# Kernel optimization log

Measured on AMD Instinct MI355X. Metric: run time of the kernel, lower is better.

## Reference

```python
import jax, jax.numpy as jnp
import numpy as np

B, S, H, D = 2, 2048, 16, 128

def setup_inputs() -> dict:
    key = jax.random.key(0)
    kq, kk, kv = jax.random.split(key, 3)
    q = jax.random.normal(kq, (B, S, H, D), dtype=jnp.float32)
    k = jax.random.normal(kk, (B, S, H, D), dtype=jnp.float32)
    v = jax.random.normal(kv, (B, S, H, D), dtype=jnp.float32)
    return {"q": q, "k": k, "v": v}

def reference(q, k, v):
    # Flash-attention semantics: layout [B, S, H, D], causal mask,
    # softmax_scale = 1/sqrt(head_dim), no dropout/window/alibi/bias.
    scale = 1.0 / jnp.sqrt(jnp.asarray(q.shape[-1], dtype=q.dtype))
    # scores: [B, H, Sq, Sk]
    scores = jnp.einsum("bqhd,bkhd->bhqk", q, k) * scale
    sq, sk = q.shape[1], k.shape[1]
    causal_mask = jnp.arange(sk)[None, :] <= jnp.arange(sq)[:, None]  # [Sq, Sk]
    scores = jnp.where(causal_mask[None, None, :, :], scores, jnp.finfo(scores.dtype).min)
    probs = jax.nn.softmax(scores, axis=-1)
    out = jnp.einsum("bhqk,bkhd->bqhd", probs, v)
    return out
```

## Files before the change

kernel.cpp:

```cpp
#include <hip/hip_runtime.h>
#include <hip/hip_bf16.h>

namespace {

constexpr int Bn = 2, Sn = 2048, Hn = 16, Dn = 128;
constexpr int QBLK = 128;
constexpr int KVBLK = 32;
constexpr int RS = Hn * Dn;
constexpr float QSCALE = 0.08838834764831845f * 1.4426950408889634f;

constexpr size_t IMG_BYTES = (size_t)Bn * Hn * 64 * 8192;
constexpr size_t WS_NEED   = 2 * IMG_BYTES;

typedef __bf16 bf16x8 __attribute__((ext_vector_type(8)));
typedef __bf16 bf16x4 __attribute__((ext_vector_type(4)));
typedef float  f32x16 __attribute__((ext_vector_type(16)));

__device__ __forceinline__ f32x16 mfma32(bf16x8 a, bf16x8 b, f32x16 c) {
  return __builtin_amdgcn_mfma_f32_32x32x16_bf16(a, b, c, 0, 0, 0);
}
__device__ __forceinline__ unsigned pack2(float a, float b) {
  union { __bf16 h[2]; unsigned u; } r;
  r.h[0] = (__bf16)a; r.h[1] = (__bf16)b;
  return r.u;
}
__device__ __forceinline__ float pair_max(float x, int hi) {
  auto r = __builtin_amdgcn_permlane32_swap(__float_as_uint(x), __float_as_uint(x), false, false);
  const float sw = __uint_as_float(hi ? r[0] : r[1]);
  return fmaxf(x, sw);
}
__device__ __forceinline__ float pair_sum(float x, int hi) {
  auto r = __builtin_amdgcn_permlane32_swap(__float_as_uint(x), __float_as_uint(x), false, false);
  const float sw = __uint_as_float(hi ? r[0] : r[1]);
  return x + sw;
}
__device__ __forceinline__ float f4e(const float4& v, int j) {
  return j == 0 ? v.x : j == 1 ? v.y : j == 2 ? v.z : v.w;
}
__device__ __forceinline__ float lane_bcast(int row, float v) {
  return __uint_as_float(__builtin_amdgcn_ds_bpermute(row * 4, __float_as_uint(v)));
}

__device__ __forceinline__ void cp16(const char* g, char* l) {
  __builtin_amdgcn_global_load_lds(
      (const __attribute__((address_space(1))) void*)g,
      (__attribute__((address_space(3))) void*)l, 16, 0, 0);
}

__device__ __forceinline__ void dma_barrier() {
  __builtin_amdgcn_sched_barrier(0);
  asm volatile("s_waitcnt vmcnt(0) lgkmcnt(0)" ::: "memory");
  __builtin_amdgcn_s_barrier();
  __builtin_amdgcn_sched_barrier(0);
}
__device__ __forceinline__ void pipeline_barrier() {
  __builtin_amdgcn_sched_barrier(0);
  asm volatile("s_waitcnt lgkmcnt(0)" ::: "memory");
  __builtin_amdgcn_s_barrier();
  __builtin_amdgcn_sched_barrier(0);
}

__global__ __launch_bounds__(256)
void prep_kv(const float* __restrict__ K, const float* __restrict__ V,
             __bf16* __restrict__ KI, __bf16* __restrict__ VI)
{
  const int gid  = (int)blockIdx.x * 256 + (int)threadIdx.x;
  const int half = gid >> 20;
  const int id   = gid & ((1 << 20) - 1);
  const int chunk = id >> 9;
  const int rem   = id & 511;
  const int bh = chunk >> 6, c = chunk & 63;
  const int b = bh >> 4, h = bh & 15;
  if (half == 0) {
    const int key = rem >> 4, dblk = rem & 15;
    const float* src = K + ((size_t)b * Sn + (size_t)c * 32 + key) * RS + h * Dn + dblk * 8;
    float4 a  = *(const float4*)src;
    float4 c2 = *(const float4*)(src + 4);
    bf16x8 f;
    f[0] = (__bf16)a.x;  f[1] = (__bf16)a.y;  f[2] = (__bf16)a.z;  f[3] = (__bf16)a.w;
    f[4] = (__bf16)c2.x; f[5] = (__bf16)c2.y; f[6] = (__bf16)c2.z; f[7] = (__bf16)c2.w;
    char* dst = (char*)KI + (size_t)chunk * 8192 + ((key * 256 + dblk * 16) ^ ((key & 7) << 4));
    *(bf16x8*)dst = f;
  } else {
    const int d = rem >> 2, koct = rem & 3;
    const float* src = V + ((size_t)b * Sn + (size_t)c * 32 + koct * 8) * RS + h * Dn + d;
    bf16x8 f;
#pragma unroll
    for (int j = 0; j < 8; ++j) f[j] = (__bf16)src[(size_t)j * RS];
    const int off = (d * 64 + koct * 16) ^ ((d & 3) << 4) ^ (((d >> 3) & 1) << 6);
    *(bf16x8*)((char*)VI + (size_t)chunk * 8192 + off) = f;
  }
}

__global__ __launch_bounds__(512)
void fa_fwd_dma(const float* __restrict__ Q, const __bf16* __restrict__ KI,
                const __bf16* __restrict__ VI, float* __restrict__ O)
{
  __shared__ __align__(16) __bf16 Klds[4][4096];
  __shared__ __align__(16) __bf16 Vt[4][4096];

  const int tid  = threadIdx.x;
  const int lane = tid & 63;
  const int wave = tid >> 6;
  const int col  = lane & 31;
  const int hi   = lane >> 5;
  const int grp  = wave >> 2;
  const int wq   = wave & 3;

  const int xcd  = (int)blockIdx.x & 7;
  const int s    = (int)blockIdx.x >> 3;
  const int qt   = s & 15;
  const int hidx = xcd * 4 + (s >> 4);
  const int b    = hidx >> 4, h = hidx & 15;
  const int q0w  = qt * QBLK + wq * 32;
  const int T    = 2 * (qt + 1);
  const size_t base = ((size_t)b * Sn) * RS + (size_t)h * Dn;

  const char* KIc = (const char*)KI + (size_t)hidx * 64 * 8192;
  const char* VIc = (const char*)VI + (size_t)hidx * 64 * 8192;

  const int sr = wave >> 1;
  const int hb = (wave & 1) * 4096;
  auto stageK2 = [&](int ss) {
    if (sr < 2) {
      const int ck = 2 * ss + sr;
      const char* g = KIc + (size_t)ck * 8192 + hb;
      char* l = (char*)&Klds[ck & 3][0] + hb;
#pragma unroll
      for (int i = 0; i < 4; ++i) cp16(g + i * 1024 + lane * 16, l + i * 1024);
    }
  };
  auto stageV2 = [&](int ss) {
    if (sr >= 2) {
      const int cv = 2 * ss + (sr - 2);
      const char* g = VIc + (size_t)cv * 8192 + hb;
      char* l = (char*)&Vt[cv & 3][0] + hb;
#pragma unroll
      for (int i = 0; i < 4; ++i) cp16(g + i * 1024 + lane * 16, l + i * 1024);
    }
  };

  const int cswz = (col & 7) << 4;
  const int vswz = ((col & 3) << 4) ^ (((col >> 3) & 1) << 6);

  bf16x8 qf[8];
  {
    const float* qp = Q + base + (size_t)(q0w + col) * RS + hi * 8;
#pragma unroll
    for (int kk = 0; kk < 8; ++kk) {
      float4 a = *(const float4*)(qp + kk * 16);
      float4 c2 = *(const float4*)(qp + kk * 16 + 4);
      bf16x8 f;
      f[0] = (__bf16)(a.x * QSCALE);  f[1] = (__bf16)(a.y * QSCALE);
      f[2] = (__bf16)(a.z * QSCALE);  f[3] = (__bf16)(a.w * QSCALE);
      f[4] = (__bf16)(c2.x * QSCALE); f[5] = (__bf16)(c2.y * QSCALE);
      f[6] = (__bf16)(c2.z * QSCALE); f[7] = (__bf16)(c2.w * QSCALE);
      qf[kk] = f;
    }
  }

  f32x16 o0 = {}, o1 = {}, o2 = {}, o3 = {};
  float m = -1e30f, l = 0.f;

  stageK2(0);
  stageV2(0);
  stageK2(1);
  dma_barrier();

  f32x16 st_cur = {};
  if (grp * KVBLK <= q0w + 31) {
    const char* kb = (const char*)&Klds[grp][0];
    __builtin_amdgcn_s_setprio(1);
#pragma unroll
    for (int kk = 0; kk < 8; ++kk) {
      bf16x8 ka = *(const bf16x8*)(kb + ((col * 256 + kk * 32 + hi * 16) ^ cswz));
      st_cur = mfma32(ka, qf[kk], st_cur);
    }
    __builtin_amdgcn_s_setprio(0);
  }
  dma_barrier();

#pragma unroll 1
  for (int t = 0; t < T; ++t) {
    if (t + 2 < T) stageK2(t + 2);
    if (t + 1 < T) stageV2(t + 1);

    f32x16 stn = {};
    const int icn = 2 * (t + 1) + grp;
    if (t + 1 < T && icn * KVBLK <= q0w + 31) {
      const char* kb = (const char*)&Klds[icn & 3][0];
      __builtin_amdgcn_s_setprio(1);
#pragma unroll
      for (int kk = 0; kk < 8; ++kk) {
        bf16x8 ka = *(const bf16x8*)(kb + ((col * 256 + kk * 32 + hi * 16) ^ cswz));
        stn = mfma32(ka, qf[kk], stn);
      }
      __builtin_amdgcn_s_setprio(0);
    }

    const int kv0 = (2 * t + grp) * KVBLK;
    if (kv0 <= q0w + 31) {
      if (kv0 + KVBLK - 1 > q0w) {
        const int qk = q0w + col - kv0;
#pragma unroll
        for (int r = 0; r < 16; ++r) {
          const int krow = (r & 3) + 8 * (r >> 2) + 4 * hi;
          st_cur[r] = (krow <= qk) ? st_cur[r] : -1e30f;
        }
      }

      float t8[8];
#pragma unroll
      for (int r = 0; r < 8; ++r) t8[r] = fmaxf(st_cur[r], st_cur[r + 8]);
#pragma unroll
      for (int r = 0; r < 4; ++r) t8[r] = fmaxf(t8[r], t8[r + 4]);
      const float pmax = pair_max(fmaxf(fmaxf(t8[0], t8[1]), fmaxf(t8[2], t8[3])), hi);

      if (!__all(pmax <= m + 11.0f)) {
        const float mnew = fmaxf(m, pmax);
        const float al = __builtin_amdgcn_exp2f(m - mnew);
        m = mnew;
        l *= al;
#pragma unroll
        for (int r = 0; r < 16; ++r) {
          const int row = (r & 3) + 8 * (r >> 2) + 4 * hi;
          const float ar = lane_bcast(row, al);
          o0[r] *= ar; o1[r] *= ar; o2[r] *= ar; o3[r] *= ar;
        }
      }

      float s4[4] = {0.f, 0.f, 0.f, 0.f};
#pragma unroll
      for (int r = 0; r < 16; ++r) {
        st_cur[r] = __builtin_amdgcn_exp2f(st_cur[r] - m);
        s4[r & 3] += st_cur[r];
      }
      l += pair_sum((s4[0] + s4[1]) + (s4[2] + s4[3]), hi);

      unsigned cw[8];
#pragma unroll
      for (int i = 0; i < 8; ++i) cw[i] = pack2(st_cur[2 * i], st_cur[2 * i + 1]);
      union { unsigned u[4]; bf16x8 v; } pa0, pa1;
      {
        auto s02 = __builtin_amdgcn_permlane32_swap(cw[0], cw[2], false, false);
        auto s13 = __builtin_amdgcn_permlane32_swap(cw[1], cw[3], false, false);
        auto s46 = __builtin_amdgcn_permlane32_swap(cw[4], cw[6], false, false);
        auto s57 = __builtin_amdgcn_permlane32_swap(cw[5], cw[7], false, false);
        pa0.u[0] = s02[0]; pa0.u[2] = s02[1];
        pa0.u[1] = s13[0]; pa0.u[3] = s13[1];
        pa1.u[0] = s46[0]; pa1.u[2] = s46[1];
        pa1.u[1] = s57[0]; pa1.u[3] = s57[1];
      }

      const char* vb = (const char*)&Vt[(2 * t + grp) & 3][0];
      __builtin_amdgcn_s_setprio(1);
#pragma unroll
      for (int ks = 0; ks < 2; ++ks) {
        const bf16x8 pa = ks ? pa1.v : pa0.v;
#define PV_STEP(ovar, dt) { \
        bf16x8 vf = *(const bf16x8*)(vb + ((((dt)*32 + col) * 64 + ks * 32 + hi * 16) ^ vswz)); \
        ovar = mfma32(pa, vf, ovar); }
        PV_STEP(o0, 0) PV_STEP(o1, 1) PV_STEP(o2, 2) PV_STEP(o3, 3)
#undef PV_STEP
      }
      __builtin_amdgcn_s_setprio(0);
    }
    dma_barrier();
    st_cur = stn;
  }

  float* ob  = reinterpret_cast<float*>(&Klds[0][0]);
  float* mlb = reinterpret_cast<float*>(&Vt[0][0]);
  if (grp == 1) {
    mlb[wq * 128 + lane] = m;
    mlb[wq * 128 + 64 + lane] = l;
#pragma unroll
    for (int r = 0; r < 16; ++r) {
      ob[wq * 1024 + r * 64 + lane] = o0[r];
      ob[4096 + wq * 1024 + r * 64 + lane] = o1[r];
    }
  }
  __syncthreads();
  float f0 = 1.f, f1 = 0.f;
  if (grp == 0) {
    const float m1 = mlb[wq * 128 + lane];
    const float l1 = mlb[wq * 128 + 64 + lane];
    const float mS = fmaxf(m, m1);
    f0 = __builtin_amdgcn_exp2f(m - mS);
    f1 = __builtin_amdgcn_exp2f(m1 - mS);
    l = l * f0 + l1 * f1;
#pragma unroll
    for (int r = 0; r < 16; ++r) {
      const int row = (r & 3) + 8 * (r >> 2) + 4 * hi;
      const float a0 = lane_bcast(row, f0), a1 = lane_bcast(row, f1);
      o0[r] = o0[r] * a0 + ob[wq * 1024 + r * 64 + lane] * a1;
      o1[r] = o1[r] * a0 + ob[4096 + wq * 1024 + r * 64 + lane] * a1;
    }
  }
  __syncthreads();
  if (grp == 1) {
#pragma unroll
    for (int r = 0; r < 16; ++r) {
      ob[wq * 1024 + r * 64 + lane] = o2[r];
      ob[4096 + wq * 1024 + r * 64 + lane] = o3[r];
    }
  }
  __syncthreads();
  if (grp == 0) {
#pragma unroll
    for (int r = 0; r < 16; ++r) {
      const int row = (r & 3) + 8 * (r >> 2) + 4 * hi;
      const float a0 = lane_bcast(row, f0), a1 = lane_bcast(row, f1);
      o2[r] = o2[r] * a0 + ob[wq * 1024 + r * 64 + lane] * a1;
      o3[r] = o3[r] * a0 + ob[4096 + wq * 1024 + r * 64 + lane] * a1;
    }
    const float linv = 1.0f / l;
#pragma unroll
    for (int r = 0; r < 16; ++r) {
      const int row = (r & 3) + 8 * (r >> 2) + 4 * hi;
      const float lr = lane_bcast(row, linv);
      float* op = O + base + (size_t)(q0w + row) * RS + col;
      op[0]  = o0[r] * lr;
      op[32] = o1[r] * lr;
      op[64] = o2[r] * lr;
      op[96] = o3[r] * lr;
    }
  }
}

__global__ __launch_bounds__(512)
void fa_fwd_reg(const float* __restrict__ Q, const float* __restrict__ K,
                const float* __restrict__ V, float* __restrict__ O)
{
  __shared__ __align__(16) __bf16 Klds[6][KVBLK * 128];
  __shared__ __align__(16) __bf16 Vt[4][128 * KVBLK];

  const int tid  = threadIdx.x;
  const int lane = tid & 63;
  const int wave = tid >> 6;
  const int col  = lane & 31;
  const int hi   = lane >> 5;
  const int grp  = wave >> 2;
  const int wq   = wave & 3;

  const int xcd  = (int)blockIdx.x & 7;
  const int s    = (int)blockIdx.x >> 3;
  const int hidx = xcd * 4 + (s & 3);
  const int b    = hidx >> 4, h = hidx & 15;
  const int s2   = s >> 2;
  const int qt   = (s < 32) ? (15 - s2) : (s2 - 8);
  const int q0w  = qt * QBLK + wq * 32;
  const int T    = 2 * (qt + 1);
  const size_t base = ((size_t)b * Sn) * RS + (size_t)h * Dn;

  const int sthalf = tid >> 8, ht = tid & 255;
  const int skey = ht >> 3, sd = (ht & 7) * 16;
  const int vkey4 = (ht & 7) * 4, vd4 = (ht >> 3) * 4;

  float4 kr[4], vr[4];
  auto loadK = [&](int ss) {
    const int kv0 = (2 * ss + sthalf) * KVBLK;
    const float* kp = K + base + (size_t)(kv0 + skey) * RS + sd;
#pragma unroll
    for (int i = 0; i < 4; ++i) kr[i] = *(const float4*)(kp + 4 * i);
  };
  auto loadV = [&](int ss) {
    const int kv0 = (2 * ss + sthalf) * KVBLK;
    const float* vp = V + base + (size_t)(kv0 + vkey4) * RS + vd4;
#pragma unroll
    for (int i = 0; i < 4; ++i) vr[i] = *(const float4*)(vp + (size_t)i * RS);
  };
  auto stageK = [&](int ss) {
    char* kb = (char*)&Klds[(2 * ss + sthalf) % 6][0];
    const int kbase = skey * 256 + sd * 2;
    const int kswz  = (skey & 7) << 4;
#pragma unroll
    for (int i = 0; i < 2; ++i) {
      bf16x8 f;
      f[0] = (__bf16)kr[2*i].x;   f[1] = (__bf16)kr[2*i].y;
      f[2] = (__bf16)kr[2*i].z;   f[3] = (__bf16)kr[2*i].w;
      f[4] = (__bf16)kr[2*i+1].x; f[5] = (__bf16)kr[2*i+1].y;
      f[6] = (__bf16)kr[2*i+1].z; f[7] = (__bf16)kr[2*i+1].w;
      *(bf16x8*)(kb + ((kbase + 16 * i) ^ kswz)) = f;
    }
  };
  auto stageV = [&](int ss) {
    char* vb = (char*)&Vt[(2 * ss + sthalf) & 3][0];
    const int b6 = ((vd4 >> 3) & 1) << 6;
#pragma unroll
    for (int j = 0; j < 4; ++j) {
      bf16x4 w;
      w[0] = (__bf16)f4e(vr[0], j);
      w[1] = (__bf16)f4e(vr[1], j);
      w[2] = (__bf16)f4e(vr[2], j);
      w[3] = (__bf16)f4e(vr[3], j);
      const int addr = (((vd4 + j) * 64 + vkey4 * 2) ^ (j << 4)) ^ b6;
      *(bf16x4*)(vb + addr) = w;
    }
  };

  const int cswz = (col & 7) << 4;
  const int vswz = ((col & 3) << 4) ^ (((col >> 3) & 1) << 6);

  bf16x8 qf[8];
  {
    const float* qp = Q + base + (size_t)(q0w + col) * RS + hi * 8;
#pragma unroll
    for (int kk = 0; kk < 8; ++kk) {
      float4 a = *(const float4*)(qp + kk * 16);
      float4 c2 = *(const float4*)(qp + kk * 16 + 4);
      bf16x8 f;
      f[0] = (__bf16)(a.x * QSCALE);  f[1] = (__bf16)(a.y * QSCALE);
      f[2] = (__bf16)(a.z * QSCALE);  f[3] = (__bf16)(a.w * QSCALE);
      f[4] = (__bf16)(c2.x * QSCALE); f[5] = (__bf16)(c2.y * QSCALE);
      f[6] = (__bf16)(c2.z * QSCALE); f[7] = (__bf16)(c2.w * QSCALE);
      qf[kk] = f;
    }
  }

  f32x16 o0 = {}, o1 = {}, o2 = {}, o3 = {};
  float m = -1e30f, l = 0.f;

  loadK(0); loadV(0);
  stageK(0);
  loadK(1);
  stageV(0);
  loadV(1);
  stageK(1);
  if (2 < T) loadK(2);
  pipeline_barrier();

  f32x16 st_cur = {};
  if (grp * KVBLK <= q0w + 31) {
    const char* kb = (const char*)&Klds[grp][0];
    __builtin_amdgcn_s_setprio(1);
#pragma unroll
    for (int kk = 0; kk < 8; ++kk) {
      bf16x8 ka = *(const bf16x8*)(kb + ((col * 256 + kk * 32 + hi * 16) ^ cswz));
      st_cur = mfma32(ka, qf[kk], st_cur);
    }
    __builtin_amdgcn_s_setprio(0);
  }

#pragma unroll 1
  for (int t = 0; t < T; ++t) {
    f32x16 stn = {};
    const int icn = 2 * (t + 1) + grp;
    if (t + 1 < T && icn * KVBLK <= q0w + 31) {
      const char* kb = (const char*)&Klds[icn % 6][0];
      __builtin_amdgcn_s_setprio(1);
#pragma unroll
      for (int kk = 0; kk < 8; ++kk) {
        bf16x8 ka = *(const bf16x8*)(kb + ((col * 256 + kk * 32 + hi * 16) ^ cswz));
        stn = mfma32(ka, qf[kk], stn);
      }
      __builtin_amdgcn_s_setprio(0);
    }

    if (t + 2 < T) stageK(t + 2);
    if (t + 1 < T) stageV(t + 1);
    if (t + 3 < T) loadK(t + 3);
    if (t + 2 < T) loadV(t + 2);

    const int kv0 = (2 * t + grp) * KVBLK;
    if (kv0 <= q0w + 31) {
      if (kv0 + KVBLK - 1 > q0w) {
        const int qk = q0w + col - kv0;
#pragma unroll
        for (int r = 0; r < 16; ++r) {
          const int krow = (r & 3) + 8 * (r >> 2) + 4 * hi;
          st_cur[r] = (krow <= qk) ? st_cur[r] : -1e30f;
        }
      }

      float t8[8];
#pragma unroll
      for (int r = 0; r < 8; ++r) t8[r] = fmaxf(st_cur[r], st_cur[r + 8]);
#pragma unroll
      for (int r = 0; r < 4; ++r) t8[r] = fmaxf(t8[r], t8[r + 4]);
      const float pmax = pair_max(fmaxf(fmaxf(t8[0], t8[1]), fmaxf(t8[2], t8[3])), hi);

      if (!__all(pmax <= m + 11.0f)) {
        const float mnew = fmaxf(m, pmax);
        const float al = __builtin_amdgcn_exp2f(m - mnew);
        m = mnew;
        l *= al;
#pragma unroll
        for (int r = 0; r < 16; ++r) {
          const int row = (r & 3) + 8 * (r >> 2) + 4 * hi;
          const float ar = lane_bcast(row, al);
          o0[r] *= ar; o1[r] *= ar; o2[r] *= ar; o3[r] *= ar;
        }
      }

      float s4[4] = {0.f, 0.f, 0.f, 0.f};
#pragma unroll
      for (int r = 0; r < 16; ++r) {
        st_cur[r] = __builtin_amdgcn_exp2f(st_cur[r] - m);
        s4[r & 3] += st_cur[r];
      }
      l += pair_sum((s4[0] + s4[1]) + (s4[2] + s4[3]), hi);

      unsigned cw[8];
#pragma unroll
      for (int i = 0; i < 8; ++i) cw[i] = pack2(st_cur[2 * i], st_cur[2 * i + 1]);
      union { unsigned u[4]; bf16x8 v; } pa0, pa1;
      {
        auto s02 = __builtin_amdgcn_permlane32_swap(cw[0], cw[2], false, false);
        auto s13 = __builtin_amdgcn_permlane32_swap(cw[1], cw[3], false, false);
        auto s46 = __builtin_amdgcn_permlane32_swap(cw[4], cw[6], false, false);
        auto s57 = __builtin_amdgcn_permlane32_swap(cw[5], cw[7], false, false);
        pa0.u[0] = s02[0]; pa0.u[2] = s02[1];
        pa0.u[1] = s13[0]; pa0.u[3] = s13[1];
        pa1.u[0] = s46[0]; pa1.u[2] = s46[1];
        pa1.u[1] = s57[0]; pa1.u[3] = s57[1];
      }

      const char* vb = (const char*)&Vt[(2 * t + grp) & 3][0];
      __builtin_amdgcn_s_setprio(1);
#pragma unroll
      for (int ks = 0; ks < 2; ++ks) {
        const bf16x8 pa = ks ? pa1.v : pa0.v;
#define PV_STEP(ovar, dt) { \
        bf16x8 vf = *(const bf16x8*)(vb + ((((dt)*32 + col) * 64 + ks * 32 + hi * 16) ^ vswz)); \
        ovar = mfma32(pa, vf, ovar); }
        PV_STEP(o0, 0) PV_STEP(o1, 1) PV_STEP(o2, 2) PV_STEP(o3, 3)
#undef PV_STEP
      }
      __builtin_amdgcn_s_setprio(0);
    }
    pipeline_barrier();
    st_cur = stn;
  }

  float* ob  = reinterpret_cast<float*>(&Klds[0][0]);
  float* mlb = reinterpret_cast<float*>(&Vt[0][0]);
  if (grp == 1) {
    mlb[wq * 128 + lane] = m;
    mlb[wq * 128 + 64 + lane] = l;
#pragma unroll
    for (int r = 0; r < 16; ++r) {
      ob[wq * 1024 + r * 64 + lane] = o0[r];
      ob[4096 + wq * 1024 + r * 64 + lane] = o1[r];
    }
  }
  __syncthreads();
  float f0 = 1.f, f1 = 0.f;
  if (grp == 0) {
    const float m1 = mlb[wq * 128 + lane];
    const float l1 = mlb[wq * 128 + 64 + lane];
    const float mS = fmaxf(m, m1);
    f0 = __builtin_amdgcn_exp2f(m - mS);
    f1 = __builtin_amdgcn_exp2f(m1 - mS);
    l = l * f0 + l1 * f1;
#pragma unroll
    for (int r = 0; r < 16; ++r) {
      const int row = (r & 3) + 8 * (r >> 2) + 4 * hi;
      const float a0 = lane_bcast(row, f0), a1 = lane_bcast(row, f1);
      o0[r] = o0[r] * a0 + ob[wq * 1024 + r * 64 + lane] * a1;
      o1[r] = o1[r] * a0 + ob[4096 + wq * 1024 + r * 64 + lane] * a1;
    }
  }
  __syncthreads();
  if (grp == 1) {
#pragma unroll
    for (int r = 0; r < 16; ++r) {
      ob[wq * 1024 + r * 64 + lane] = o2[r];
      ob[4096 + wq * 1024 + r * 64 + lane] = o3[r];
    }
  }
  __syncthreads();
  if (grp == 0) {
#pragma unroll
    for (int r = 0; r < 16; ++r) {
      const int row = (r & 3) + 8 * (r >> 2) + 4 * hi;
      const float a0 = lane_bcast(row, f0), a1 = lane_bcast(row, f1);
      o2[r] = o2[r] * a0 + ob[wq * 1024 + r * 64 + lane] * a1;
      o3[r] = o3[r] * a0 + ob[4096 + wq * 1024 + r * 64 + lane] * a1;
    }
    const float linv = 1.0f / l;
#pragma unroll
    for (int r = 0; r < 16; ++r) {
      const int row = (r & 3) + 8 * (r >> 2) + 4 * hi;
      const float lr = lane_bcast(row, linv);
      float* op = O + base + (size_t)(q0w + row) * RS + col;
      op[0]  = o0[r] * lr;
      op[32] = o1[r] * lr;
      op[64] = o2[r] * lr;
      op[96] = o3[r] * lr;
    }
  }
}

}

extern "C" void kernel_launch(void* const* d_in, const int* , int ,
                              void* d_out, int , void* d_ws, size_t ws_size,
                              hipStream_t stream) {
  const float* q = (const float*)d_in[0];
  const float* k = (const float*)d_in[1];
  const float* v = (const float*)d_in[2];
  float* o = (float*)d_out;
  if (d_ws != nullptr && ws_size >= WS_NEED) {
    __bf16* ki = (__bf16*)d_ws;
    __bf16* vi = (__bf16*)((char*)d_ws + IMG_BYTES);
    hipLaunchKernelGGL(prep_kv, dim3(8192), dim3(256), 0, stream, k, v, ki, vi);
    hipLaunchKernelGGL(fa_fwd_dma, dim3(512), dim3(512), 0, stream, q, ki, vi, o);
  } else {
    hipLaunchKernelGGL(fa_fwd_reg, dim3(512), dim3(512), 0, stream, q, k, v, o);
  }
}
```

Measured before the change: 120.8 us.

## Split KV across four wave groups with paired causal q-tiles per block

Replaces the DMA attention kernel with a variant where each block owns 64 query rows, handles two query tiles (a long one and a short one) to balance causal work, and splits each 128-key step across four wave groups of two waves, each with its own KV chunk. Each step stages four K and four V chunks at once, then the four partial softmax states are merged through LDS in a two-level reduction. The goal is better load balance across blocks and more independent MFMA work per step. In exchange it drops the software-pipelined QK prefetch, adds a barrier around every stage, and adds extra merge passes through LDS.

```diff
diff --git a/kernel.cpp b/kernel.cpp
--- a/kernel.cpp
+++ b/kernel.cpp
@@ -93,11 +93,278 @@
 }
 
 __global__ __launch_bounds__(512)
-void fa_fwd_dma(const float* __restrict__ Q, const __bf16* __restrict__ KI,
-                const __bf16* __restrict__ VI, float* __restrict__ O)
+void fa_fwd_dma4(const float* __restrict__ Q, const __bf16* __restrict__ KI,
+                 const __bf16* __restrict__ VI, float* __restrict__ O)
 {
   __shared__ __align__(16) __bf16 Klds[4][4096];
   __shared__ __align__(16) __bf16 Vt[4][4096];
+
+  const int tid  = threadIdx.x;
+  const int lane = tid & 63;
+  const int wave = tid >> 6;
+  const int col  = lane & 31;
+  const int hi   = lane >> 5;
+  const int grp  = wave >> 1;
+  const int wq   = wave & 1;
+
+  const int xcd  = (int)blockIdx.x & 7;
+  const int s    = (int)blockIdx.x >> 3;
+  const int h2   = s & 3;
+  const int pp   = (s >> 2) & 7;
+  const int half = (s >> 5) & 1;
+  const int hidx = xcd * 4 + h2;
+  const int b    = hidx >> 4, h = hidx & 15;
+  const size_t base = ((size_t)b * Sn) * RS + (size_t)h * Dn;
+
+  const char* KIc = (const char*)KI + (size_t)hidx * 64 * 8192;
+  const char* VIc = (const char*)VI + (size_t)hidx * 64 * 8192;
+
+  auto stageSS = [&](int ss) {
+    const int c = 4 * ss + (wave & 3);
+    const char* g = (wave < 4 ? KIc : VIc) + (size_t)c * 8192 + lane * 16;
+    char* l = (char*)(wave < 4 ? &Klds[wave & 3][0] : &Vt[wave & 3][0]);
+#pragma unroll
+    for (int i = 0; i < 8; ++i) cp16(g + i * 1024, l + i * 1024);
+  };
+
+  const int cswz = (col & 7) << 4;
+  const int vswz = ((col & 3) << 4) ^ (((col >> 3) & 1) << 6);
+
+#pragma unroll 1
+  for (int tp = 0; tp < 2; ++tp) {
+    const int qt  = tp ? pp : (15 - pp);
+    const int T   = qt + 1;
+    const int q0w = qt * QBLK + half * 64 + wq * 32;
+
+    bf16x8 qf[8];
+    {
+      const float* qp = Q + base + (size_t)(q0w + col) * RS + hi * 8;
+#pragma unroll
+      for (int kk = 0; kk < 8; ++kk) {
+        float4 a = *(const float4*)(qp + kk * 16);
+        float4 c2 = *(const float4*)(qp + kk * 16 + 4);
+        bf16x8 f;
+        f[0] = (__bf16)(a.x * QSCALE);  f[1] = (__bf16)(a.y * QSCALE);
+        f[2] = (__bf16)(a.z * QSCALE);  f[3] = (__bf16)(a.w * QSCALE);
+        f[4] = (__bf16)(c2.x * QSCALE); f[5] = (__bf16)(c2.y * QSCALE);
+        f[6] = (__bf16)(c2.z * QSCALE); f[7] = (__bf16)(c2.w * QSCALE);
+        qf[kk] = f;
+      }
+    }
+
+    f32x16 o0 = {}, o1 = {}, o2 = {}, o3 = {};
+    float m = -1e30f, l = 0.f;
+
+    stageSS(0);
+    dma_barrier();
+
+#pragma unroll 1
+    for (int t = 0; t < T; ++t) {
+      const int cc  = 4 * t + grp;
+      const int kv0 = cc * 32;
+      if (kv0 <= q0w + 31) {
+        f32x16 st = {};
+        {
+          const char* kb = (const char*)&Klds[grp][0];
+          __builtin_amdgcn_s_setprio(1);
+#pragma unroll
+          for (int kk = 0; kk < 8; ++kk) {
+            bf16x8 ka = *(const bf16x8*)(kb + ((col * 256 + kk * 32 + hi * 16) ^ cswz));
+            st = mfma32(ka, qf[kk], st);
+          }
+          __builtin_amdgcn_s_setprio(0);
+        }
+
+        if (kv0 + KVBLK - 1 > q0w) {
+          const int qk = q0w + col - kv0;
+#pragma unroll
+          for (int r = 0; r < 16; ++r) {
+            const int krow = (r & 3) + 8 * (r >> 2) + 4 * hi;
+            st[r] = (krow <= qk) ? st[r] : -1e30f;
+          }
+        }
+
+        float t8[8];
+#pragma unroll
+        for (int r = 0; r < 8; ++r) t8[r] = fmaxf(st[r], st[r + 8]);
+#pragma unroll
+        for (int r = 0; r < 4; ++r) t8[r] = fmaxf(t8[r], t8[r + 4]);
+        const float pmax = pair_max(fmaxf(fmaxf(t8[0], t8[1]), fmaxf(t8[2], t8[3])), hi);
+
+        if (!__all(pmax <= m + 11.0f)) {
+          const float mnew = fmaxf(m, pmax);
+          const float al = __builtin_amdgcn_exp2f(m - mnew);
+          m = mnew;
+          l *= al;
+#pragma unroll
+          for (int r = 0; r < 16; ++r) {
+            const int row = (r & 3) + 8 * (r >> 2) + 4 * hi;
+            const float ar = lane_bcast(row, al);
+            o0[r] *= ar; o1[r] *= ar; o2[r] *= ar; o3[r] *= ar;
+          }
+        }
+
+        float s4[4] = {0.f, 0.f, 0.f, 0.f};
+#pragma unroll
+        for (int r = 0; r < 16; ++r) {
+          st[r] = __builtin_amdgcn_exp2f(st[r] - m);
+          s4[r & 3] += st[r];
+        }
+        l += pair_sum((s4[0] + s4[1]) + (s4[2] + s4[3]), hi);
+
+        unsigned cw[8];
+#pragma unroll
+        for (int i = 0; i < 8; ++i) cw[i] = pack2(st[2 * i], st[2 * i + 1]);
+        union { unsigned u[4]; bf16x8 v; } pa0, pa1;
+        {
+          auto s02 = __builtin_amdgcn_permlane32_swap(cw[0], cw[2], false, false);
+          auto s13 = __builtin_amdgcn_permlane32_swap(cw[1], cw[3], false, false);
+          auto s46 = __builtin_amdgcn_permlane32_swap(cw[4], cw[6], false, false);
+          auto s57 = __builtin_amdgcn_permlane32_swap(cw[5], cw[7], false, false);
+          pa0.u[0] = s02[0]; pa0.u[2] = s02[1];
+          pa0.u[1] = s13[0]; pa0.u[3] = s13[1];
+          pa1.u[0] = s46[0]; pa1.u[2] = s46[1];
+          pa1.u[1] = s57[0]; pa1.u[3] = s57[1];
+        }
+
+        const char* vb = (const char*)&Vt[grp][0];
+        __builtin_amdgcn_s_setprio(1);
+#pragma unroll
+        for (int ks = 0; ks < 2; ++ks) {
+          const bf16x8 pa = ks ? pa1.v : pa0.v;
+#define PV_STEP(ovar, dt) { \
+          bf16x8 vf = *(const bf16x8*)(vb + ((((dt)*32 + col) * 64 + ks * 32 + hi * 16) ^ vswz)); \
+          ovar = mfma32(pa, vf, ovar); }
+          PV_STEP(o0, 0) PV_STEP(o1, 1) PV_STEP(o2, 2) PV_STEP(o3, 3)
+#undef PV_STEP
+        }
+        __builtin_amdgcn_s_setprio(0);
+      }
+
+      pipeline_barrier();
+      if (t + 1 < T) stageSS(t + 1);
+      dma_barrier();
+    }
+
+    float* ob  = reinterpret_cast<float*>(&Klds[0][0]);
+    float* mlb = reinterpret_cast<float*>(&Vt[0][0]);
+    float f0 = 1.f, f1 = 0.f;
+    {
+      const int src = grp & 1;
+      float* obr = ob  + (grp >> 1) * 4096;
+      float* mlr = mlb + (grp >> 1) * 256;
+      if (src) {
+        mlr[wq * 128 + lane] = m;
+        mlr[wq * 128 + 64 + lane] = l;
+#pragma unroll
+        for (int r = 0; r < 16; ++r) {
+          obr[wq * 1024 + r * 64 + lane] = o0[r];
+          obr[2048 + wq * 1024 + r * 64 + lane] = o1[r];
+        }
+      }
+      __syncthreads();
+      if (!src) {
+        const float m1 = mlr[wq * 128 + lane];
+        const float l1 = mlr[wq * 128 + 64 + lane];
+        const float mS = fmaxf(m, m1);
+        f0 = __builtin_amdgcn_exp2f(m - mS);
+        f1 = __builtin_amdgcn_exp2f(m1 - mS);
+        m = mS;
+        l = l * f0 + l1 * f1;
+#pragma unroll
+        for (int r = 0; r < 16; ++r) {
+          const int row = (r & 3) + 8 * (r >> 2) + 4 * hi;
+          const float a0 = lane_bcast(row, f0), a1 = lane_bcast(row, f1);
+          o0[r] = o0[r] * a0 + obr[wq * 1024 + r * 64 + lane] * a1;
+          o1[r] = o1[r] * a0 + obr[2048 + wq * 1024 + r * 64 + lane] * a1;
+        }
+      }
+      __syncthreads();
+      if (src) {
+#pragma unroll
+        for (int r = 0; r < 16; ++r) {
+          obr[wq * 1024 + r * 64 + lane] = o2[r];
+          obr[2048 + wq * 1024 + r * 64 + lane] = o3[r];
+        }
+      }
+      __syncthreads();
+      if (!src) {
+#pragma unroll
+        for (int r = 0; r < 16; ++r) {
+          const int row = (r & 3) + 8 * (r >> 2) + 4 * hi;
+          const float a0 = lane_bcast(row, f0), a1 = lane_bcast(row, f1);
+          o2[r] = o2[r] * a0 + obr[wq * 1024 + r * 64 + lane] * a1;
+          o3[r] = o3[r] * a0 + obr[2048 + wq * 1024 + r * 64 + lane] * a1;
+        }
+      }
+      __syncthreads();
+    }
+    {
+      if (grp == 2) {
+        mlb[wq * 128 + lane] = m;
+        mlb[wq * 128 + 64 + lane] = l;
+#pragma unroll
+        for (int r = 0; r < 16; ++r) {
+          ob[wq * 1024 + r * 64 + lane] = o0[r];
+          ob[2048 + wq * 1024 + r * 64 + lane] = o1[r];
+        }
+      }
+      __syncthreads();
+      if (grp == 0) {
+        const float m1 = mlb[wq * 128 + lane];
+        const float l1 = mlb[wq * 128 + 64 + lane];
+        const float mS = fmaxf(m, m1);
+        f0 = __builtin_amdgcn_exp2f(m - mS);
+        f1 = __builtin_amdgcn_exp2f(m1 - mS);
+        l = l * f0 + l1 * f1;
+#pragma unroll
+        for (int r = 0; r < 16; ++r) {
+          const int row = (r & 3) + 8 * (r >> 2) + 4 * hi;
+          const float a0 = lane_bcast(row, f0), a1 = lane_bcast(row, f1);
+          o0[r] = o0[r] * a0 + ob[wq * 1024 + r * 64 + lane] * a1;
+          o1[r] = o1[r] * a0 + ob[2048 + wq * 1024 + r * 64 + lane] * a1;
+        }
+      }
+      __syncthreads();
+      if (grp == 2) {
+#pragma unroll
+        for (int r = 0; r < 16; ++r) {
+          ob[wq * 1024 + r * 64 + lane] = o2[r];
+          ob[2048 + wq * 1024 + r * 64 + lane] = o3[r];
+        }
+      }
+      __syncthreads();
+      if (grp == 0) {
+#pragma unroll
+        for (int r = 0; r < 16; ++r) {
+          const int row = (r & 3) + 8 * (r >> 2) + 4 * hi;
+          const float a0 = lane_bcast(row, f0), a1 = lane_bcast(row, f1);
+          o2[r] = o2[r] * a0 + ob[wq * 1024 + r * 64 + lane] * a1;
+          o3[r] = o3[r] * a0 + ob[2048 + wq * 1024 + r * 64 + lane] * a1;
+        }
+        const float linv = 1.0f / l;
+#pragma unroll
+        for (int r = 0; r < 16; ++r) {
+          const int row = (r & 3) + 8 * (r >> 2) + 4 * hi;
+          const float lr = lane_bcast(row, linv);
+          float* op = O + base + (size_t)(q0w + row) * RS + col;
+          op[0]  = o0[r] * lr;
+          op[32] = o1[r] * lr;
+          op[64] = o2[r] * lr;
+          op[96] = o3[r] * lr;
+        }
+      }
+    }
+    __syncthreads();
+  }
+}
+
+__global__ __launch_bounds__(512)
+void fa_fwd_reg(const float* __restrict__ Q, const float* __restrict__ K,
+                const float* __restrict__ V, float* __restrict__ O)
+{
+  __shared__ __align__(16) __bf16 Klds[6][KVBLK * 128];
+  __shared__ __align__(16) __bf16 Vt[4][128 * KVBLK];
 
   const int tid  = threadIdx.x;
   const int lane = tid & 63;
@@ -109,34 +376,57 @@
 
   const int xcd  = (int)blockIdx.x & 7;
   const int s    = (int)blockIdx.x >> 3;
-  const int qt   = s & 15;
-  const int hidx = xcd * 4 + (s >> 4);
+  const int hidx = xcd * 4 + (s & 3);
   const int b    = hidx >> 4, h = hidx & 15;
+  const int s2   = s >> 2;
+  const int qt   = (s < 32) ? (15 - s2) : (s2 - 8);
   const int q0w  = qt * QBLK + wq * 32;
   const int T    = 2 * (qt + 1);
   const size_t base = ((size_t)b * Sn) * RS + (size_t)h * Dn;
 
-  const char* KIc = (const char*)KI + (size_t)hidx * 64 * 8192;
-  const char* VIc = (const char*)VI + (size_t)hidx * 64 * 8192;
-
-  const int sr = wave >> 1;
-  const int hb = (wave & 1) * 4096;
-  auto stageK2 = [&](int ss) {
-    if (sr < 2) {
-      const int ck = 2 * ss + sr;
-      const char* g = KIc + (size_t)ck * 8192 + hb;
-      char* l = (char*)&Klds[ck & 3][0] + hb;
-#pragma unroll
-      for (int i = 0; i < 4; ++i) cp16(g + i * 1024 + lane * 16, l + i * 1024);
-    }
+  const int sthalf = tid >> 8, ht = tid & 255;
+  const int skey = ht >> 3, sd = (ht & 7) * 16;
+  const int vkey4 = (ht & 7) * 4, vd4 = (ht >> 3) * 4;
+
+  float4 kr[4], vr[4];
+  auto loadK = [&](int ss) {
+    const int kv0 = (2 * ss + sthalf) * KVBLK;
+    const float* kp = K + base + (size_t)(kv0 + skey) * RS + sd;
+#pragma unroll
+    for (int i = 0; i < 4; ++i) kr[i] = *(const float4*)(kp + 4 * i);
   };
-  auto stageV2 = [&](int ss) {
-    if (sr >= 2) {
-      const int cv = 2 * ss + (sr - 2);
-      const char* g = VIc + (size_t)cv * 8192 + hb;
-      char* l = (char*)&Vt[cv & 3][0] + hb;
-#pragma unroll
-      for (int i = 0; i < 4; ++i) cp16(g + i * 1024 + lane * 16, l + i * 1024);
+  auto loadV = [&](int ss) {
+    const int kv0 = (2 * ss + sthalf) * KVBLK;
+    const float* vp = V + base + (size_t)(kv0 + vkey4) * RS + vd4;
+#pragma unroll
+    for (int i = 0; i < 4; ++i) vr[i] = *(const float4*)(vp + (size_t)i * RS);
+  };
+  auto stageK = [&](int ss) {
+    char* kb = (char*)&Klds[(2 * ss + sthalf) % 6][0];
+    const int kbase = skey * 256 + sd * 2;
+    const int kswz  = (skey & 7) << 4;
+#pragma unroll
+    for (int i = 0; i < 2; ++i) {
+      bf16x8 f;
+      f[0] = (__bf16)kr[2*i].x;   f[1] = (__bf16)kr[2*i].y;
+      f[2] = (__bf16)kr[2*i].z;   f[3] = (__bf16)kr[2*i].w;
+      f[4] = (__bf16)kr[2*i+1].x; f[5] = (__bf16)kr[2*i+1].y;
+      f[6] = (__bf16)kr[2*i+1].z; f[7] = (__bf16)kr[2*i+1].w;
+      *(bf16x8*)(kb + ((kbase + 16 * i) ^ kswz)) = f;
+    }
+  };
+  auto stageV = [&](int ss) {
+    char* vb = (char*)&Vt[(2 * ss + sthalf) & 3][0];
+    const int b6 = ((vd4 >> 3) & 1) << 6;
+#pragma unroll
+    for (int j = 0; j < 4; ++j) {
+      bf16x4 w;
+      w[0] = (__bf16)f4e(vr[0], j);
+      w[1] = (__bf16)f4e(vr[1], j);
+      w[2] = (__bf16)f4e(vr[2], j);
+      w[3] = (__bf16)f4e(vr[3], j);
+      const int addr = (((vd4 + j) * 64 + vkey4 * 2) ^ (j << 4)) ^ b6;
+      *(bf16x4*)(vb + addr) = w;
     }
   };
 
@@ -162,10 +452,14 @@
   f32x16 o0 = {}, o1 = {}, o2 = {}, o3 = {};
   float m = -1e30f, l = 0.f;
 
-  stageK2(0);
-  stageV2(0);
-  stageK2(1);
-  dma_barrier();
+  loadK(0); loadV(0);
+  stageK(0);
+  loadK(1);
+  stageV(0);
+  loadV(1);
+  stageK(1);
+  if (2 < T) loadK(2);
+  pipeline_barrier();
 
   f32x16 st_cur = {};
   if (grp * KVBLK <= q0w + 31) {
@@ -178,17 +472,13 @@
     }
     __builtin_amdgcn_s_setprio(0);
   }
-  dma_barrier();
 
 #pragma unroll 1
   for (int t = 0; t < T; ++t) {
-    if (t + 2 < T) stageK2(t + 2);
-    if (t + 1 < T) stageV2(t + 1);
-
     f32x16 stn = {};
     const int icn = 2 * (t + 1) + grp;
     if (t + 1 < T && icn * KVBLK <= q0w + 31) {
-      const char* kb = (const char*)&Klds[icn & 3][0];
+      const char* kb = (const char*)&Klds[icn % 6][0];
       __builtin_amdgcn_s_setprio(1);
 #pragma unroll
       for (int kk = 0; kk < 8; ++kk) {
@@ -197,6 +487,11 @@
       }
       __builtin_amdgcn_s_setprio(0);
     }
+
+    if (t + 2 < T) stageK(t + 2);
+    if (t + 1 < T) stageV(t + 1);
+    if (t + 3 < T) loadK(t + 3);
+    if (t + 2 < T) loadV(t + 2);
 
     const int kv0 = (2 * t + grp) * KVBLK;
     if (kv0 <= q0w + 31) {
@@ -265,270 +560,6 @@
       }
       __builtin_amdgcn_s_setprio(0);
     }
-    dma_barrier();
-    st_cur = stn;
-  }
-
-  float* ob  = reinterpret_cast<float*>(&Klds[0][0]);
-  float* mlb = reinterpret_cast<float*>(&Vt[0][0]);
-  if (grp == 1) {
-    mlb[wq * 128 + lane] = m;
-    mlb[wq * 128 + 64 + lane] = l;
-#pragma unroll
-    for (int r = 0; r < 16; ++r) {
-      ob[wq * 1024 + r * 64 + lane] = o0[r];
-      ob[4096 + wq * 1024 + r * 64 + lane] = o1[r];
-    }
-  }
-  __syncthreads();
-  float f0 = 1.f, f1 = 0.f;
-  if (grp == 0) {
-    const float m1 = mlb[wq * 128 + lane];
-    const float l1 = mlb[wq * 128 + 64 + lane];
-    const float mS = fmaxf(m, m1);
-    f0 = __builtin_amdgcn_exp2f(m - mS);
-    f1 = __builtin_amdgcn_exp2f(m1 - mS);
-    l = l * f0 + l1 * f1;
-#pragma unroll
-    for (int r = 0; r < 16; ++r) {
-      const int row = (r & 3) + 8 * (r >> 2) + 4 * hi;
-      const float a0 = lane_bcast(row, f0), a1 = lane_bcast(row, f1);
-      o0[r] = o0[r] * a0 + ob[wq * 1024 + r * 64 + lane] * a1;
-      o1[r] = o1[r] * a0 + ob[4096 + wq * 1024 + r * 64 + lane] * a1;
-    }
-  }
-  __syncthreads();
-  if (grp == 1) {
-#pragma unroll
-    for (int r = 0; r < 16; ++r) {
-      ob[wq * 1024 + r * 64 + lane] = o2[r];
-      ob[4096 + wq * 1024 + r * 64 + lane] = o3[r];
-    }
-  }
-  __syncthreads();
-  if (grp == 0) {
-#pragma unroll
-    for (int r = 0; r < 16; ++r) {
-      const int row = (r & 3) + 8 * (r >> 2) + 4 * hi;
-      const float a0 = lane_bcast(row, f0), a1 = lane_bcast(row, f1);
-      o2[r] = o2[r] * a0 + ob[wq * 1024 + r * 64 + lane] * a1;
-      o3[r] = o3[r] * a0 + ob[4096 + wq * 1024 + r * 64 + lane] * a1;
-    }
-    const float linv = 1.0f / l;
-#pragma unroll
-    for (int r = 0; r < 16; ++r) {
-      const int row = (r & 3) + 8 * (r >> 2) + 4 * hi;
-      const float lr = lane_bcast(row, linv);
-      float* op = O + base + (size_t)(q0w + row) * RS + col;
-      op[0]  = o0[r] * lr;
-      op[32] = o1[r] * lr;
-      op[64] = o2[r] * lr;
-      op[96] = o3[r] * lr;
-    }
-  }
-}
-
-__global__ __launch_bounds__(512)
-void fa_fwd_reg(const float* __restrict__ Q, const float* __restrict__ K,
-                const float* __restrict__ V, float* __restrict__ O)
-{
-  __shared__ __align__(16) __bf16 Klds[6][KVBLK * 128];
-  __shared__ __align__(16) __bf16 Vt[4][128 * KVBLK];
-
-  const int tid  = threadIdx.x;
-  const int lane = tid & 63;
-  const int wave = tid >> 6;
-  const int col  = lane & 31;
-  const int hi   = lane >> 5;
-  const int grp  = wave >> 2;
-  const int wq   = wave & 3;
-
-  const int xcd  = (int)blockIdx.x & 7;
-  const int s    = (int)blockIdx.x >> 3;
-  const int hidx = xcd * 4 + (s & 3);
-  const int b    = hidx >> 4, h = hidx & 15;
-  const int s2   = s >> 2;
-  const int qt   = (s < 32) ? (15 - s2) : (s2 - 8);
-  const int q0w  = qt * QBLK + wq * 32;
-  const int T    = 2 * (qt + 1);
-  const size_t base = ((size_t)b * Sn) * RS + (size_t)h * Dn;
-
-  const int sthalf = tid >> 8, ht = tid & 255;
-  const int skey = ht >> 3, sd = (ht & 7) * 16;
-  const int vkey4 = (ht & 7) * 4, vd4 = (ht >> 3) * 4;
-
-  float4 kr[4], vr[4];
-  auto loadK = [&](int ss) {
-    const int kv0 = (2 * ss + sthalf) * KVBLK;
-    const float* kp = K + base + (size_t)(kv0 + skey) * RS + sd;
-#pragma unroll
-    for (int i = 0; i < 4; ++i) kr[i] = *(const float4*)(kp + 4 * i);
-  };
-  auto loadV = [&](int ss) {
-    const int kv0 = (2 * ss + sthalf) * KVBLK;
-    const float* vp = V + base + (size_t)(kv0 + vkey4) * RS + vd4;
-#pragma unroll
-    for (int i = 0; i < 4; ++i) vr[i] = *(const float4*)(vp + (size_t)i * RS);
-  };
-  auto stageK = [&](int ss) {
-    char* kb = (char*)&Klds[(2 * ss + sthalf) % 6][0];
-    const int kbase = skey * 256 + sd * 2;
-    const int kswz  = (skey & 7) << 4;
-#pragma unroll
-    for (int i = 0; i < 2; ++i) {
-      bf16x8 f;
-      f[0] = (__bf16)kr[2*i].x;   f[1] = (__bf16)kr[2*i].y;
-      f[2] = (__bf16)kr[2*i].z;   f[3] = (__bf16)kr[2*i].w;
-      f[4] = (__bf16)kr[2*i+1].x; f[5] = (__bf16)kr[2*i+1].y;
-      f[6] = (__bf16)kr[2*i+1].z; f[7] = (__bf16)kr[2*i+1].w;
-      *(bf16x8*)(kb + ((kbase + 16 * i) ^ kswz)) = f;
-    }
-  };
-  auto stageV = [&](int ss) {
-    char* vb = (char*)&Vt[(2 * ss + sthalf) & 3][0];
-    const int b6 = ((vd4 >> 3) & 1) << 6;
-#pragma unroll
-    for (int j = 0; j < 4; ++j) {
-      bf16x4 w;
-      w[0] = (__bf16)f4e(vr[0], j);
-      w[1] = (__bf16)f4e(vr[1], j);
-      w[2] = (__bf16)f4e(vr[2], j);
-      w[3] = (__bf16)f4e(vr[3], j);
-      const int addr = (((vd4 + j) * 64 + vkey4 * 2) ^ (j << 4)) ^ b6;
-      *(bf16x4*)(vb + addr) = w;
-    }
-  };
-
-  const int cswz = (col & 7) << 4;
-  const int vswz = ((col & 3) << 4) ^ (((col >> 3) & 1) << 6);
-
-  bf16x8 qf[8];
-  {
-    const float* qp = Q + base + (size_t)(q0w + col) * RS + hi * 8;
-#pragma unroll
-    for (int kk = 0; kk < 8; ++kk) {
-      float4 a = *(const float4*)(qp + kk * 16);
-      float4 c2 = *(const float4*)(qp + kk * 16 + 4);
-      bf16x8 f;
-      f[0] = (__bf16)(a.x * QSCALE);  f[1] = (__bf16)(a.y * QSCALE);
-      f[2] = (__bf16)(a.z * QSCALE);  f[3] = (__bf16)(a.w * QSCALE);
-      f[4] = (__bf16)(c2.x * QSCALE); f[5] = (__bf16)(c2.y * QSCALE);
-      f[6] = (__bf16)(c2.z * QSCALE); f[7] = (__bf16)(c2.w * QSCALE);
-      qf[kk] = f;
-    }
-  }
-
-  f32x16 o0 = {}, o1 = {}, o2 = {}, o3 = {};
-  float m = -1e30f, l = 0.f;
-
-  loadK(0); loadV(0);
-  stageK(0);
-  loadK(1);
-  stageV(0);
-  loadV(1);
-  stageK(1);
-  if (2 < T) loadK(2);
-  pipeline_barrier();
-
-  f32x16 st_cur = {};
-  if (grp * KVBLK <= q0w + 31) {
-    const char* kb = (const char*)&Klds[grp][0];
-    __builtin_amdgcn_s_setprio(1);
-#pragma unroll
-    for (int kk = 0; kk < 8; ++kk) {
-      bf16x8 ka = *(const bf16x8*)(kb + ((col * 256 + kk * 32 + hi * 16) ^ cswz));
-      st_cur = mfma32(ka, qf[kk], st_cur);
-    }
-    __builtin_amdgcn_s_setprio(0);
-  }
-
-#pragma unroll 1
-  for (int t = 0; t < T; ++t) {
-    f32x16 stn = {};
-    const int icn = 2 * (t + 1) + grp;
-    if (t + 1 < T && icn * KVBLK <= q0w + 31) {
-      const char* kb = (const char*)&Klds[icn % 6][0];
-      __builtin_amdgcn_s_setprio(1);
-#pragma unroll
-      for (int kk = 0; kk < 8; ++kk) {
-        bf16x8 ka = *(const bf16x8*)(kb + ((col * 256 + kk * 32 + hi * 16) ^ cswz));
-        stn = mfma32(ka, qf[kk], stn);
-      }
-      __builtin_amdgcn_s_setprio(0);
-    }
-
-    if (t + 2 < T) stageK(t + 2);
-    if (t + 1 < T) stageV(t + 1);
-    if (t + 3 < T) loadK(t + 3);
-    if (t + 2 < T) loadV(t + 2);
-
-    const int kv0 = (2 * t + grp) * KVBLK;
-    if (kv0 <= q0w + 31) {
-      if (kv0 + KVBLK - 1 > q0w) {
-        const int qk = q0w + col - kv0;
-#pragma unroll
-        for (int r = 0; r < 16; ++r) {
-          const int krow = (r & 3) + 8 * (r >> 2) + 4 * hi;
-          st_cur[r] = (krow <= qk) ? st_cur[r] : -1e30f;
-        }
-      }
-
-      float t8[8];
-#pragma unroll
-      for (int r = 0; r < 8; ++r) t8[r] = fmaxf(st_cur[r], st_cur[r + 8]);
-#pragma unroll
-      for (int r = 0; r < 4; ++r) t8[r] = fmaxf(t8[r], t8[r + 4]);
-      const float pmax = pair_max(fmaxf(fmaxf(t8[0], t8[1]), fmaxf(t8[2], t8[3])), hi);
-
-      if (!__all(pmax <= m + 11.0f)) {
-        const float mnew = fmaxf(m, pmax);
-        const float al = __builtin_amdgcn_exp2f(m - mnew);
-        m = mnew;
-        l *= al;
-#pragma unroll
-        for (int r = 0; r < 16; ++r) {
-          const int row = (r & 3) + 8 * (r >> 2) + 4 * hi;
-          const float ar = lane_bcast(row, al);
-          o0[r] *= ar; o1[r] *= ar; o2[r] *= ar; o3[r] *= ar;
-        }
-      }
-
-      float s4[4] = {0.f, 0.f, 0.f, 0.f};
-#pragma unroll
-      for (int r = 0; r < 16; ++r) {
-        st_cur[r] = __builtin_amdgcn_exp2f(st_cur[r] - m);
-        s4[r & 3] += st_cur[r];
-      }
-      l += pair_sum((s4[0] + s4[1]) + (s4[2] + s4[3]), hi);
-
-      unsigned cw[8];
-#pragma unroll
-      for (int i = 0; i < 8; ++i) cw[i] = pack2(st_cur[2 * i], st_cur[2 * i + 1]);
-      union { unsigned u[4]; bf16x8 v; } pa0, pa1;
-      {
-        auto s02 = __builtin_amdgcn_permlane32_swap(cw[0], cw[2], false, false);
-        auto s13 = __builtin_amdgcn_permlane32_swap(cw[1], cw[3], false, false);
-        auto s46 = __builtin_amdgcn_permlane32_swap(cw[4], cw[6], false, false);
-        auto s57 = __builtin_amdgcn_permlane32_swap(cw[5], cw[7], false, false);
-        pa0.u[0] = s02[0]; pa0.u[2] = s02[1];
-        pa0.u[1] = s13[0]; pa0.u[3] = s13[1];
-        pa1.u[0] = s46[0]; pa1.u[2] = s46[1];
-        pa1.u[1] = s57[0]; pa1.u[3] = s57[1];
-      }
-
-      const char* vb = (const char*)&Vt[(2 * t + grp) & 3][0];
-      __builtin_amdgcn_s_setprio(1);
-#pragma unroll
-      for (int ks = 0; ks < 2; ++ks) {
-        const bf16x8 pa = ks ? pa1.v : pa0.v;
-#define PV_STEP(ovar, dt) { \
-        bf16x8 vf = *(const bf16x8*)(vb + ((((dt)*32 + col) * 64 + ks * 32 + hi * 16) ^ vswz)); \
-        ovar = mfma32(pa, vf, ovar); }
-        PV_STEP(o0, 0) PV_STEP(o1, 1) PV_STEP(o2, 2) PV_STEP(o3, 3)
-#undef PV_STEP
-      }
-      __builtin_amdgcn_s_setprio(0);
-    }
     pipeline_barrier();
     st_cur = stn;
   }
@@ -605,7 +636,7 @@
     __bf16* ki = (__bf16*)d_ws;
     __bf16* vi = (__bf16*)((char*)d_ws + IMG_BYTES);
     hipLaunchKernelGGL(prep_kv, dim3(8192), dim3(256), 0, stream, k, v, ki, vi);
-    hipLaunchKernelGGL(fa_fwd_dma, dim3(512), dim3(512), 0, stream, q, ki, vi, o);
+    hipLaunchKernelGGL(fa_fwd_dma4, dim3(512), dim3(512), 0, stream, q, ki, vi, o);
   } else {
     hipLaunchKernelGGL(fa_fwd_reg, dim3(512), dim3(512), 0, stream, q, k, v, o);
   }
```

Measured after the change: 116.1 us. -3.9%, faster.
